# Optimization experiments

Measured on AMD Instinct MI355X. Metric: run time of the kernel, lower is better.

The kernel has to match this reference:

```python
import jax, jax.numpy as jnp
import numpy as np

C = 4  # n_features_per_level
RES = [128, 256, 512, 1024]  # base_resolution=128, per_level_scale=2, n_levels=4


def grid_sample(grid, pts):
    """Bilinear grid_sample, align_corners=False, zero padding.
    grid: (B, C, H, W); pts: (B, N, 2) with pts[...,0]=x (width), pts[...,1]=y (height).
    Returns (B, C, N)."""
    B, Cc, H, W = grid.shape
    fx = (pts[..., 0] + 1.0) * 0.5 * W - 0.5
    fy = (pts[..., 1] + 1.0) * 0.5 * H - 0.5
    x0 = jnp.floor(fx)
    y0 = jnp.floor(fy)
    wx = (fx - x0)[:, None, :]
    wy = (fy - y0)[:, None, :]
    x0 = x0.astype(jnp.int32)
    y0 = y0.astype(jnp.int32)

    def corner(xi, yi):
        valid = ((xi >= 0) & (xi < W) & (yi >= 0) & (yi < H)).astype(grid.dtype)
        xc = jnp.clip(xi, 0, W - 1)
        yc = jnp.clip(yi, 0, H - 1)
        vals = jax.vmap(lambda g, yy, xx: g[:, yy, xx])(grid, yc, xc)  # (B, C, N)
        return vals * valid[:, None, :]

    v00 = corner(x0, y0)
    v10 = corner(x0 + 1, y0)
    v01 = corner(x0, y0 + 1)
    v11 = corner(x0 + 1, y0 + 1)
    return (v00 * (1 - wx) * (1 - wy) + v10 * wx * (1 - wy)
            + v01 * (1 - wx) * wy + v11 * wx * wy)


def _flat(f):
    # (3, C, N) -> (N, 3*C), matching torch out.reshape(3*C, N).T
    return f.reshape(3 * f.shape[1], f.shape[2]).T


def _forward(x, triplanes, trilines):
    x2 = x * 2.0 - 1.0  # map [0,1] -> [-1,1]
    # plane projections: (xz), (yx), (zy)
    x_pl = jnp.stack([
        jnp.stack([x2[:, 0], x2[:, 2]], -1),
        jnp.stack([x2[:, 1], x2[:, 0]], -1),
        jnp.stack([x2[:, 2], x2[:, 1]], -1)], 0)  # (3, N, 2)
    x_li = jnp.stack([x2[:, 0], x2[:, 1], x2[:, 2]], 0)
    x_li = jnp.stack([x_li, jnp.zeros_like(x_li)], -1)  # (3, N, 2)
    feats = []
    for tp, tl in zip(triplanes, trilines):
        f = _flat(grid_sample(tp, x_pl)) * _flat(grid_sample(tl, x_li))  # (N, 3C)
        feats.append(f)
    return jnp.concatenate(feats, -1)  # (N, 3*C*n_levels)


def setup_inputs() -> dict:
    key = jax.random.key(0)
    ks = jax.random.split(key, 9)
    N = 1 << 20
    d = {"x": jax.random.uniform(ks[0], (N, 3), jnp.float32)}
    for i, r in enumerate(RES):
        d[f"triplane_{i}"] = jax.random.normal(ks[1 + i], (3, C, r, r), jnp.float32)
        d[f"triline_{i}"] = jax.random.normal(ks[5 + i], (3, C, r, 1), jnp.float32)
    return d


def reference(x, triplane_0, triplane_1, triplane_2, triplane_3,
              triline_0, triline_1, triline_2, triline_3):
    triplanes = [triplane_0, triplane_1, triplane_2, triplane_3]
    trilines = [triline_0, triline_1, triline_2, triline_3]
    return _forward(x, triplanes, trilines)
```

## Files before the change

### kernel.cpp

```cpp
#include <hip/hip_runtime.h>
#include <cstdint>


typedef float f32x4 __attribute__((ext_vector_type(4)));

static constexpr int LVL_OFF[4] = {0, 196608, 983040, 4128768};
static constexpr int S_OFF = 16711680;
static constexpr size_t WS_NEED = (size_t)(S_OFF + 48) * sizeof(float);
static constexpr int TEXELS = 4177920;

__global__ __launch_bounds__(256) void repack_all(
        const float* __restrict__ tp0, const float* __restrict__ tp1,
        const float* __restrict__ tp2, const float* __restrict__ tp3,
        const float* __restrict__ tl0, const float* __restrict__ tl1,
        const float* __restrict__ tl2, const float* __restrict__ tl3,
        float* __restrict__ ws) {
    int t = blockIdx.x * 256 + threadIdx.x;
    const float* src; int rr_shift, texoff;
    if (t < 49152)        { src = tp0; rr_shift = 14; texoff = 0; }
    else if (t < 245760)  { src = tp1; rr_shift = 16; texoff = 49152; }
    else if (t < 1032192) { src = tp2; rr_shift = 18; texoff = 245760; }
    else                  { src = tp3; rr_shift = 20; texoff = 1032192; }
    int local = t - texoff;
    int p  = local >> rr_shift;
    int yx = local & ((1 << rr_shift) - 1);
    const float* s0 = src + ((size_t)(p << 2) << rr_shift) + yx;
    float4 o;
    o.x = s0[0];
    o.y = s0[(size_t)1 << rr_shift];
    o.z = s0[(size_t)2 << rr_shift];
    o.w = s0[(size_t)3 << rr_shift];
    reinterpret_cast<float4*>(ws)[t] = o;
    if (t < 48) {
        int ll = t / 12, rem = t % 12, pp = rem >> 2, cc = rem & 3;
        const float* tl = (ll == 0) ? tl0 : (ll == 1) ? tl1 : (ll == 2) ? tl2 : tl3;
        int r = 128 << ll;
        const float* row = tl + (size_t)((pp << 2) + cc) * r;
        int y0 = (r >> 1) - 1;
        ws[S_OFF + t] = 0.5f * row[y0] + 0.5f * row[y0 + 1];
    }
}

struct BilinW {
    int i00, i10, i01, i11;
    float w00, w10, w01, w11;
};

__device__ __forceinline__ BilinW bilin_weights(int r, float u, float v) {
    float fr = (float)r;
    float fx = (u + 1.0f) * 0.5f * fr - 0.5f;
    float fy = (v + 1.0f) * 0.5f * fr - 0.5f;
    float x0f = floorf(fx), y0f = floorf(fy);
    float wx = fx - x0f, wy = fy - y0f;
    int x0 = (int)x0f, y0 = (int)y0f;
    int x1 = x0 + 1, y1 = y0 + 1;
    float vx0 = ((unsigned)x0 < (unsigned)r) ? 1.0f : 0.0f;
    float vx1 = ((unsigned)x1 < (unsigned)r) ? 1.0f : 0.0f;
    float vy0 = ((unsigned)y0 < (unsigned)r) ? 1.0f : 0.0f;
    float vy1 = ((unsigned)y1 < (unsigned)r) ? 1.0f : 0.0f;
    int x0c = min(max(x0, 0), r - 1), x1c = min(max(x1, 0), r - 1);
    int y0c = min(max(y0, 0), r - 1), y1c = min(max(y1, 0), r - 1);
    BilinW b;
    b.i00 = y0c * r + x0c; b.i10 = y0c * r + x1c;
    b.i01 = y1c * r + x0c; b.i11 = y1c * r + x1c;
    b.w00 = (1.0f - wx) * (1.0f - wy) * vx0 * vy0;
    b.w10 = wx * (1.0f - wy) * vx1 * vy0;
    b.w01 = (1.0f - wx) * wy * vx0 * vy1;
    b.w11 = wx * wy * vx1 * vy1;
    return b;
}

__device__ __forceinline__ float line_w(float t) {
    float fx = (t + 1.0f) * 0.5f - 0.5f;
    float x0f = floorf(fx);
    float wx = fx - x0f;
    int x0 = (int)x0f;
    float w = 0.0f;
    if (x0 == 0) w += 1.0f - wx;
    if (x0 == -1) w += wx;
    return w;
}

__device__ __forceinline__ f32x4 bacc(const float4& A, const float4& B2,
                                      const float4& C2, const float4& D,
                                      const BilinW& b, const float4& s, float lw) {
    f32x4 o;
    o.x = (A.x * b.w00 + B2.x * b.w10 + C2.x * b.w01 + D.x * b.w11) * (s.x * lw);
    o.y = (A.y * b.w00 + B2.y * b.w10 + C2.y * b.w01 + D.y * b.w11) * (s.y * lw);
    o.z = (A.z * b.w00 + B2.z * b.w10 + C2.z * b.w01 + D.z * b.w11) * (s.z * lw);
    o.w = (A.w * b.w00 + B2.w * b.w10 + C2.w * b.w01 + D.w * b.w11) * (s.w * lw);
    return o;
}

template <bool VEC4OUT>
__global__ __launch_bounds__(256, 2) void tri_split4(
        const float* __restrict__ x, const float4* __restrict__ planes,
        const float* __restrict__ S, float* __restrict__ out, int N) {
    int gid = blockIdx.x * 256 + threadIdx.x;
    int n = gid >> 2;
    int l = gid & 3;
    if (n >= N) return;
    float ax = x[n * 3 + 0] * 2.0f - 1.0f;
    float ay = x[n * 3 + 1] * 2.0f - 1.0f;
    float az = x[n * 3 + 2] * 2.0f - 1.0f;
    const int r = 128 << l;
    const int rr = r * r;
    int texoff = (l == 0) ? 0 : (l == 1) ? 49152 : (l == 2) ? 245760 : 1032192;
    const float4* G0 = planes + texoff;
    const float4* G1 = G0 + rr;
    const float4* G2 = G1 + rr;
    BilinW b0 = bilin_weights(r, ax, az);
    BilinW b1 = bilin_weights(r, ay, ax);
    BilinW b2 = bilin_weights(r, az, ay);
    float4 g0a = G0[b0.i00], g0b = G0[b0.i10], g0c = G0[b0.i01], g0d = G0[b0.i11];
    float4 g1a = G1[b1.i00], g1b = G1[b1.i10], g1c = G1[b1.i01], g1d = G1[b1.i11];
    float4 g2a = G2[b2.i00], g2b = G2[b2.i10], g2c = G2[b2.i01], g2d = G2[b2.i11];
    float lw0 = line_w(ax), lw1 = line_w(ay), lw2 = line_w(az);
    const float4* S4 = reinterpret_cast<const float4*>(S);
    float4 s0 = S4[l * 3 + 0], s1 = S4[l * 3 + 1], s2 = S4[l * 3 + 2];

    f32x4 o0 = bacc(g0a, g0b, g0c, g0d, b0, s0, lw0);
    f32x4 o1 = bacc(g1a, g1b, g1c, g1d, b1, s1, lw1);
    f32x4 o2 = bacc(g2a, g2b, g2c, g2d, b2, s2, lw2);

    size_t base = (size_t)n * 48 + (size_t)l * 12;
    if (VEC4OUT) {
        f32x4* op = reinterpret_cast<f32x4*>(out + base);
        __builtin_nontemporal_store(o0, op);
        __builtin_nontemporal_store(o1, op + 1);
        __builtin_nontemporal_store(o2, op + 2);
    } else {
        out[base + 0] = o0.x; out[base + 1]  = o0.y;
        out[base + 2] = o0.z; out[base + 3]  = o0.w;
        out[base + 4] = o1.x; out[base + 5]  = o1.y;
        out[base + 6] = o1.z; out[base + 7]  = o1.w;
        out[base + 8] = o2.x; out[base + 9]  = o2.y;
        out[base + 10] = o2.z; out[base + 11] = o2.w;
    }
}

__global__ __launch_bounds__(256) void tri_direct(
        const float* __restrict__ x,
        const float* __restrict__ tp0, const float* __restrict__ tp1,
        const float* __restrict__ tp2, const float* __restrict__ tp3,
        const float* __restrict__ tl0, const float* __restrict__ tl1,
        const float* __restrict__ tl2, const float* __restrict__ tl3,
        float* __restrict__ out, int N) {
    int n = blockIdx.x * blockDim.x + threadIdx.x;
    if (n >= N) return;
    float ax = x[n * 3 + 0] * 2.0f - 1.0f;
    float ay = x[n * 3 + 1] * 2.0f - 1.0f;
    float az = x[n * 3 + 2] * 2.0f - 1.0f;
    const float U[3] = {ax, ay, az};
    const float V[3] = {az, ax, ay};
    const float LW[3] = {line_w(ax), line_w(ay), line_w(az)};
    const float* TP[4] = {tp0, tp1, tp2, tp3};
    const float* TL[4] = {tl0, tl1, tl2, tl3};

#pragma unroll
    for (int l = 0; l < 4; ++l) {
        const int r = 128 << l;
        const int rr = r * r;
        const int y0 = (r >> 1) - 1;
#pragma unroll
        for (int p = 0; p < 3; ++p) {
            const float* G = TP[l] + (size_t)(p * 4) * rr;
            BilinW b = bilin_weights(r, U[p], V[p]);
            const float w = LW[p];
#pragma unroll
            for (int c = 0; c < 4; ++c) {
                const float* Gc = G + (size_t)c * rr;
                float acc = Gc[b.i00] * b.w00 + Gc[b.i10] * b.w10 +
                            Gc[b.i01] * b.w01 + Gc[b.i11] * b.w11;
                const float* row = TL[l] + (size_t)((p << 2) + c) * r;
                float s = 0.5f * row[y0] + 0.5f * row[y0 + 1];
                out[(size_t)n * 48 + l * 12 + p * 4 + c] = acc * (s * w);
            }
        }
    }
}

extern "C" void kernel_launch(void* const* d_in, const int* in_sizes, int n_in,
                              void* d_out, int out_size, void* d_ws, size_t ws_size,
                              hipStream_t stream) {
    const float* x = (const float*)d_in[0];
    const float* tp[4];
    const float* tl[4];
    bool interleaved = (n_in >= 9) && (in_sizes[2] == 1536);
    for (int l = 0; l < 4; ++l) {
        if (interleaved) {
            tp[l] = (const float*)d_in[1 + 2 * l];
            tl[l] = (const float*)d_in[2 + 2 * l];
        } else {
            tp[l] = (const float*)d_in[1 + l];
            tl[l] = (const float*)d_in[5 + l];
        }
    }
    int N = in_sizes[0] / 3;
    float* out = (float*)d_out;

    bool ws_ok = (ws_size >= WS_NEED) && (((uintptr_t)d_ws & 15u) == 0);
    if (ws_ok) {
        float* ws = (float*)d_ws;
        repack_all<<<TEXELS / 256, 256, 0, stream>>>(
            tp[0], tp[1], tp[2], tp[3], tl[0], tl[1], tl[2], tl[3], ws);
        long long total = 4LL * N;
        int grid = (int)((total + 255) / 256);
        if (((uintptr_t)d_out & 15u) == 0) {
            tri_split4<true><<<grid, 256, 0, stream>>>(
                x, (const float4*)ws, ws + S_OFF, out, N);
        } else {
            tri_split4<false><<<grid, 256, 0, stream>>>(
                x, (const float4*)ws, ws + S_OFF, out, N);
        }
    } else {
        int grid = (N + 255) / 256;
        tri_direct<<<grid, 256, 0, stream>>>(
            x, tp[0], tp[1], tp[2], tp[3], tl[0], tl[1], tl[2], tl[3], out, N);
    }
}
```

Before: 621.4 us.

## Pre-gather bilinear quads for small levels and use one thread per plane-level

Adds a prep kernel that, for levels 0-2, stores the four corner texels of every (r+1)x(r+1) cell contiguously in 64 bytes with zero padding, so each lookup is one aligned contiguous read with no bounds checks. Level 3 keeps the plain channel-interleaved layout. The main kernel now runs 12 threads per point, one per (level, plane) pair, each writing one float4 with a nontemporal store. This costs a larger workspace and prep pass (about 4x texel storage for levels 0-2) and more threads that each reload x, in exchange for fewer scattered gathers and more parallelism.

```diff
diff --git a/kernel.cpp b/kernel.cpp
--- a/kernel.cpp
+++ b/kernel.cpp
@@ -4,10 +4,168 @@
 
 typedef float f32x4 __attribute__((ext_vector_type(4)));
 
+static constexpr int QE0 = 199692;
+static constexpr int QE1 = 992280;
+static constexpr int QE2 = 4150308;
+static constexpr int L3T = 3145728;
+static constexpr int TOTAL_SLOTS = QE2 + L3T;
+static constexpr int S_OFFF = (QE2 + L3T) * 4;
+static constexpr size_t WS1_NEED = (size_t)(S_OFFF + 48) * sizeof(float);
+
 static constexpr int LVL_OFF[4] = {0, 196608, 983040, 4128768};
-static constexpr int S_OFF = 16711680;
-static constexpr size_t WS_NEED = (size_t)(S_OFF + 48) * sizeof(float);
+static constexpr int S_OFF2 = 16711680;
+static constexpr size_t WS2_NEED = (size_t)(S_OFF2 + 48) * sizeof(float);
 static constexpr int TEXELS = 4177920;
+
+__global__ __launch_bounds__(256) void prep_all(
+        const float* __restrict__ tp0, const float* __restrict__ tp1,
+        const float* __restrict__ tp2, const float* __restrict__ tp3,
+        const float* __restrict__ tl0, const float* __restrict__ tl1,
+        const float* __restrict__ tl2, const float* __restrict__ tl3,
+        float* __restrict__ ws) {
+    int t = blockIdx.x * 256 + threadIdx.x;
+    if (t < 48) {
+        int ll = t / 12, rem = t % 12, pp = rem >> 2, cc = rem & 3;
+        const float* tl = (ll == 0) ? tl0 : (ll == 1) ? tl1 : (ll == 2) ? tl2 : tl3;
+        int r = 128 << ll;
+        const float* row = tl + (size_t)((pp << 2) + cc) * r;
+        int y0 = (r >> 1) - 1;
+        ws[S_OFFF + t] = 0.5f * row[y0] + 0.5f * row[y0 + 1];
+    }
+    if (t >= TOTAL_SLOTS) return;
+    float4* ws4 = reinterpret_cast<float4*>(ws);
+    if (t < QE2) {
+        const float* src; int lvl, base;
+        if (t < QE0)      { src = tp0; lvl = 0; base = 0; }
+        else if (t < QE1) { src = tp1; lvl = 1; base = QE0; }
+        else              { src = tp2; lvl = 2; base = QE1; }
+        int lt = t - base;
+        int q = lt >> 2, s = lt & 3;
+        int r = 128 << lvl, R = r + 1, rr_shift = 2 * (7 + lvl);
+        int RR = R * R;
+        int p   = q / RR;
+        int rem = q - p * RR;
+        int yq  = rem / R;
+        int xq  = rem - yq * R;
+        int tx = xq - 1 + (s & 1);
+        int ty = yq - 1 + (s >> 1);
+        float4 o = {0.f, 0.f, 0.f, 0.f};
+        if ((unsigned)tx < (unsigned)r && (unsigned)ty < (unsigned)r) {
+            const float* sp = src + ((size_t)(p << 2) << rr_shift) + (size_t)ty * r + tx;
+            o.x = sp[0];
+            o.y = sp[(size_t)1 << rr_shift];
+            o.z = sp[(size_t)2 << rr_shift];
+            o.w = sp[(size_t)3 << rr_shift];
+        }
+        ws4[t] = o;
+    } else {
+        int t2 = t - QE2;
+        int p  = t2 >> 20;
+        int yx = t2 & 0xFFFFF;
+        const float* sp = tp3 + ((size_t)(p << 2) << 20) + yx;
+        float4 o;
+        o.x = sp[0];
+        o.y = sp[(size_t)1 << 20];
+        o.z = sp[(size_t)2 << 20];
+        o.w = sp[(size_t)3 << 20];
+        ws4[t] = o;
+    }
+}
+
+struct BilinW {
+    int i00, i10, i01, i11;
+    float w00, w10, w01, w11;
+};
+
+__device__ __forceinline__ BilinW bilin_weights(int r, float u, float v) {
+    float fr = (float)r;
+    float fx = (u + 1.0f) * 0.5f * fr - 0.5f;
+    float fy = (v + 1.0f) * 0.5f * fr - 0.5f;
+    float x0f = floorf(fx), y0f = floorf(fy);
+    float wx = fx - x0f, wy = fy - y0f;
+    int x0 = (int)x0f, y0 = (int)y0f;
+    int x1 = x0 + 1, y1 = y0 + 1;
+    float vx0 = ((unsigned)x0 < (unsigned)r) ? 1.0f : 0.0f;
+    float vx1 = ((unsigned)x1 < (unsigned)r) ? 1.0f : 0.0f;
+    float vy0 = ((unsigned)y0 < (unsigned)r) ? 1.0f : 0.0f;
+    float vy1 = ((unsigned)y1 < (unsigned)r) ? 1.0f : 0.0f;
+    int x0c = min(max(x0, 0), r - 1), x1c = min(max(x1, 0), r - 1);
+    int y0c = min(max(y0, 0), r - 1), y1c = min(max(y1, 0), r - 1);
+    BilinW b;
+    b.i00 = y0c * r + x0c; b.i10 = y0c * r + x1c;
+    b.i01 = y1c * r + x0c; b.i11 = y1c * r + x1c;
+    b.w00 = (1.0f - wx) * (1.0f - wy) * vx0 * vy0;
+    b.w10 = wx * (1.0f - wy) * vx1 * vy0;
+    b.w01 = (1.0f - wx) * wy * vx0 * vy1;
+    b.w11 = wx * wy * vx1 * vy1;
+    return b;
+}
+
+__device__ __forceinline__ float line_w(float t) {
+    float fx = (t + 1.0f) * 0.5f - 0.5f;
+    float x0f = floorf(fx);
+    float wx = fx - x0f;
+    int x0 = (int)x0f;
+    float w = 0.0f;
+    if (x0 == 0) w += 1.0f - wx;
+    if (x0 == -1) w += wx;
+    return w;
+}
+
+template <bool VEC4OUT>
+__global__ __launch_bounds__(256) void tri12(const float* __restrict__ x,
+                                             const f32x4* __restrict__ ws4,
+                                             const float* __restrict__ S,
+                                             float* __restrict__ out, int N) {
+    int gid = blockIdx.x * 256 + threadIdx.x;
+    int n = gid / 12;
+    int k = gid - n * 12;
+    if (n >= N) return;
+    float ax = x[n * 3 + 0] * 2.0f - 1.0f;
+    float ay = x[n * 3 + 1] * 2.0f - 1.0f;
+    float az = x[n * 3 + 2] * 2.0f - 1.0f;
+    int l = k / 3;
+    int p = k - l * 3;
+    float u = (p == 0) ? ax : (p == 1) ? ay : az;
+    float v = (p == 0) ? az : (p == 1) ? ax : ay;
+    float lw = line_w(u);
+    const f32x4* S4 = reinterpret_cast<const f32x4*>(S);
+    f32x4 s = S4[k];
+
+    f32x4 o;
+    if (l < 3) {
+        int r = 128 << l, R = r + 1;
+        float fr = (float)r;
+        float fx = (u + 1.0f) * 0.5f * fr - 0.5f;
+        float fy = (v + 1.0f) * 0.5f * fr - 0.5f;
+        float x0f = floorf(fx), y0f = floorf(fy);
+        float wx = fx - x0f, wy = fy - y0f;
+        int ix = (int)x0f + 1;
+        int iy = (int)y0f + 1;
+        ix = min(max(ix, 0), R - 1);
+        iy = min(max(iy, 0), R - 1);
+        int qbase = (l == 0) ? 0 : (l == 1) ? QE0 : QE1;
+        const f32x4* Q = ws4 + qbase + (size_t)((p * R + iy) * R + ix) * 4;
+        f32x4 q0 = Q[0], q1 = Q[1], q2 = Q[2], q3 = Q[3];
+        float w00 = (1.0f - wx) * (1.0f - wy), w10 = wx * (1.0f - wy);
+        float w01 = (1.0f - wx) * wy,          w11 = wx * wy;
+        o = q0 * w00 + q1 * w10 + q2 * w01 + q3 * w11;
+    } else {
+        BilinW b = bilin_weights(1024, u, v);
+        const f32x4* G = ws4 + QE2 + (size_t)p * 1048576;
+        f32x4 g0 = G[b.i00], g1 = G[b.i10], g2 = G[b.i01], g3 = G[b.i11];
+        o = g0 * b.w00 + g1 * b.w10 + g2 * b.w01 + g3 * b.w11;
+    }
+    o = o * (s * lw);
+
+    if (VEC4OUT) {
+        __builtin_nontemporal_store(o, reinterpret_cast<f32x4*>(out) + gid);
+    } else {
+        size_t base = (size_t)gid * 4;
+        out[base + 0] = o.x; out[base + 1] = o.y;
+        out[base + 2] = o.z; out[base + 3] = o.w;
+    }
+}
 
 __global__ __launch_bounds__(256) void repack_all(
         const float* __restrict__ tp0, const float* __restrict__ tp1,
@@ -37,58 +195,18 @@
         int r = 128 << ll;
         const float* row = tl + (size_t)((pp << 2) + cc) * r;
         int y0 = (r >> 1) - 1;
-        ws[S_OFF + t] = 0.5f * row[y0] + 0.5f * row[y0 + 1];
-    }
-}
-
-struct BilinW {
-    int i00, i10, i01, i11;
-    float w00, w10, w01, w11;
-};
-
-__device__ __forceinline__ BilinW bilin_weights(int r, float u, float v) {
-    float fr = (float)r;
-    float fx = (u + 1.0f) * 0.5f * fr - 0.5f;
-    float fy = (v + 1.0f) * 0.5f * fr - 0.5f;
-    float x0f = floorf(fx), y0f = floorf(fy);
-    float wx = fx - x0f, wy = fy - y0f;
-    int x0 = (int)x0f, y0 = (int)y0f;
-    int x1 = x0 + 1, y1 = y0 + 1;
-    float vx0 = ((unsigned)x0 < (unsigned)r) ? 1.0f : 0.0f;
-    float vx1 = ((unsigned)x1 < (unsigned)r) ? 1.0f : 0.0f;
-    float vy0 = ((unsigned)y0 < (unsigned)r) ? 1.0f : 0.0f;
-    float vy1 = ((unsigned)y1 < (unsigned)r) ? 1.0f : 0.0f;
-    int x0c = min(max(x0, 0), r - 1), x1c = min(max(x1, 0), r - 1);
-    int y0c = min(max(y0, 0), r - 1), y1c = min(max(y1, 0), r - 1);
-    BilinW b;
-    b.i00 = y0c * r + x0c; b.i10 = y0c * r + x1c;
-    b.i01 = y1c * r + x0c; b.i11 = y1c * r + x1c;
-    b.w00 = (1.0f - wx) * (1.0f - wy) * vx0 * vy0;
-    b.w10 = wx * (1.0f - wy) * vx1 * vy0;
-    b.w01 = (1.0f - wx) * wy * vx0 * vy1;
-    b.w11 = wx * wy * vx1 * vy1;
-    return b;
-}
-
-__device__ __forceinline__ float line_w(float t) {
-    float fx = (t + 1.0f) * 0.5f - 0.5f;
-    float x0f = floorf(fx);
-    float wx = fx - x0f;
-    int x0 = (int)x0f;
-    float w = 0.0f;
-    if (x0 == 0) w += 1.0f - wx;
-    if (x0 == -1) w += wx;
-    return w;
+        ws[S_OFF2 + t] = 0.5f * row[y0] + 0.5f * row[y0 + 1];
+    }
 }
 
 __device__ __forceinline__ f32x4 bacc(const float4& A, const float4& B2,
                                       const float4& C2, const float4& D,
-                                      const BilinW& b, const float4& s, float lw) {
+                                      const BilinW& b, const float4& s, float lwv) {
     f32x4 o;
-    o.x = (A.x * b.w00 + B2.x * b.w10 + C2.x * b.w01 + D.x * b.w11) * (s.x * lw);
-    o.y = (A.y * b.w00 + B2.y * b.w10 + C2.y * b.w01 + D.y * b.w11) * (s.y * lw);
-    o.z = (A.z * b.w00 + B2.z * b.w10 + C2.z * b.w01 + D.z * b.w11) * (s.z * lw);
-    o.w = (A.w * b.w00 + B2.w * b.w10 + C2.w * b.w01 + D.w * b.w11) * (s.w * lw);
+    o.x = (A.x * b.w00 + B2.x * b.w10 + C2.x * b.w01 + D.x * b.w11) * (s.x * lwv);
+    o.y = (A.y * b.w00 + B2.y * b.w10 + C2.y * b.w01 + D.y * b.w11) * (s.y * lwv);
+    o.z = (A.z * b.w00 + B2.z * b.w10 + C2.z * b.w01 + D.z * b.w11) * (s.z * lwv);
+    o.w = (A.w * b.w00 + B2.w * b.w10 + C2.w * b.w01 + D.w * b.w11) * (s.w * lwv);
     return o;
 }
 
@@ -198,20 +316,34 @@
     }
     int N = in_sizes[0] / 3;
     float* out = (float*)d_out;
-
-    bool ws_ok = (ws_size >= WS_NEED) && (((uintptr_t)d_ws & 15u) == 0);
-    if (ws_ok) {
+    bool out16 = (((uintptr_t)d_out & 15u) == 0);
+
+    if (ws_size >= WS1_NEED && (((uintptr_t)d_ws & 63u) == 0)) {
+        float* ws = (float*)d_ws;
+        int prep_grid = (TOTAL_SLOTS + 255) / 256;
+        prep_all<<<prep_grid, 256, 0, stream>>>(
+            tp[0], tp[1], tp[2], tp[3], tl[0], tl[1], tl[2], tl[3], ws);
+        long long total = 12LL * N;
+        int grid = (int)((total + 255) / 256);
+        if (out16) {
+            tri12<true><<<grid, 256, 0, stream>>>(
+                x, (const f32x4*)ws, ws + S_OFFF, out, N);
+        } else {
+            tri12<false><<<grid, 256, 0, stream>>>(
+                x, (const f32x4*)ws, ws + S_OFFF, out, N);
+        }
+    } else if (ws_size >= WS2_NEED && (((uintptr_t)d_ws & 15u) == 0)) {
         float* ws = (float*)d_ws;
         repack_all<<<TEXELS / 256, 256, 0, stream>>>(
             tp[0], tp[1], tp[2], tp[3], tl[0], tl[1], tl[2], tl[3], ws);
         long long total = 4LL * N;
         int grid = (int)((total + 255) / 256);
-        if (((uintptr_t)d_out & 15u) == 0) {
+        if (out16) {
             tri_split4<true><<<grid, 256, 0, stream>>>(
-                x, (const float4*)ws, ws + S_OFF, out, N);
+                x, (const float4*)ws, ws + S_OFF2, out, N);
         } else {
             tri_split4<false><<<grid, 256, 0, stream>>>(
-                x, (const float4*)ws, ws + S_OFF, out, N);
+                x, (const float4*)ws, ws + S_OFF2, out, N);
         }
     } else {
         int grid = (N + 255) / 256;
```

New measurement: 558.3 us. 1.11x faster.
